# Performance work log

Measured on AMD Instinct MI355X. Metric: run time of the kernel, lower is better.

## Reference

```python
import jax, jax.numpy as jnp
import numpy as np

NUM_GROUPS = 64  # fixed for jit; indices are drawn in [0, 64)
H = 7
W = 7

def setup_inputs() -> dict:
    key = jax.random.key(0)
    k1, k2 = jax.random.split(key)
    x = jax.random.normal(k1, (2048, 512, 7, 7), dtype=jnp.float32)
    idx = jax.random.randint(k2, (2048,), 0, NUM_GROUPS, dtype=jnp.int32)
    return {"x": x, "tensor_list_assignmentindices": idx}

def reference(x, tensor_list_assignmentindices):
    # x: [N, M, H, W]; indices: [N] in [0, NUM_GROUPS)
    # Fused: sum over spatial dims first, then scatter-add per group.
    # Mathematically identical to scatter-then-spatial-sum in the original.
    x_sp = jnp.sum(x, axis=(2, 3))  # [N, M]
    group_sum = jax.ops.segment_sum(x_sp, tensor_list_assignmentindices,
                                    num_segments=NUM_GROUPS)  # [G, M]
    counts = jax.ops.segment_sum(jnp.ones((x.shape[0],), dtype=x.dtype),
                                 tensor_list_assignmentindices,
                                 num_segments=NUM_GROUPS)  # [G]
    out = group_sum / (counts[:, None] * (H * W))  # [G, M]
    return out[:, :, None, None]  # [G, M, 1, 1]
```

## Files before the change

kernel.cpp:

```cpp
#include <hip/hip_runtime.h>


#define N_SAMPLES 2048
#define M_CHANNELS 512
#define SPATIAL 49
#define GROUPS 64
#define SAMPLE_FLOATS (M_CHANNELS * SPATIAL)
#define WAVE_CH 64
#define WAVE_FLOATS (WAVE_CH * SPATIAL)

typedef __attribute__((address_space(1))) const void global_void;
typedef __attribute__((address_space(3))) void lds_void;

__global__ __launch_bounds__(256) void scatter_kernel(
    const float* __restrict__ x, const int* __restrict__ idx,
    float* __restrict__ accum) {
  __shared__ float lds[4 * WAVE_FLOATS];
  const int blk = blockIdx.x;
  const int n = blk >> 1;
  const int h = blk & 1;
  const int t = threadIdx.x;
  const int w = t >> 6;
  const int lane = t & 63;
  const int g = idx[n];

  const float* src = x + (size_t)n * SAMPLE_FLOATS
                       + (size_t)h * (SAMPLE_FLOATS / 2)
                       + (size_t)w * WAVE_FLOATS;
  float* ldsw = lds + w * WAVE_FLOATS;

#pragma unroll
  for (int k = 0; k < 12; ++k) {
    __builtin_amdgcn_global_load_lds(
        (global_void*)(src + (size_t)(k * 64 + lane) * 4),
        (lds_void*)(ldsw + k * 256), 16, 0, 0);
  }
  if (lane < 16) {
    __builtin_amdgcn_global_load_lds(
        (global_void*)(src + (size_t)(768 + lane) * 4),
        (lds_void*)(ldsw + 3072), 16, 0, 0);
  }

  asm volatile("s_waitcnt vmcnt(0)" ::: "memory");
  __builtin_amdgcn_sched_barrier(0);

  const float* row = ldsw + lane * SPATIAL;
  float s = 0.f;
#pragma unroll
  for (int i = 0; i < SPATIAL; ++i) s += row[i];

  atomicAdd(accum + (size_t)g * M_CHANNELS + h * (M_CHANNELS / 2)
                  + w * WAVE_CH + lane, s);
}

__global__ __launch_bounds__(512) void finalize_kernel(
    const int* __restrict__ idx, float* __restrict__ out) {
  const int g = blockIdx.x;
  const int t = threadIdx.x;

  __shared__ int cnt;
  if (t == 0) cnt = 0;
  __syncthreads();

  int local = 0;
#pragma unroll
  for (int i = 0; i < N_SAMPLES / 512; ++i)
    local += (idx[t + i * 512] == g) ? 1 : 0;
  atomicAdd(&cnt, local);
  __syncthreads();

  const float inv = 1.0f / ((float)cnt * (float)SPATIAL);
  out[(size_t)g * M_CHANNELS + t] *= inv;
}

extern "C" void kernel_launch(void* const* d_in, const int* in_sizes, int n_in,
                              void* d_out, int out_size, void* d_ws, size_t ws_size,
                              hipStream_t stream) {
  const float* x = (const float*)d_in[0];
  const int* idx = (const int*)d_in[1];
  float* out = (float*)d_out;

  hipMemsetAsync(out, 0, (size_t)GROUPS * M_CHANNELS * sizeof(float), stream);

  scatter_kernel<<<N_SAMPLES * 2, 256, 0, stream>>>(x, idx, out);
  finalize_kernel<<<GROUPS, M_CHANNELS, 0, stream>>>(idx, out);
}
```

Baseline: 278.5 us.

## Use persistent single-wave blocks with double-buffered LDS prefetch of channel chunks

Replaces the one-shot 4096-block scatter kernel with a persistent grid of 1536 single-wave blocks. Each block strides over 64-channel chunks and prefetches the next chunk into a second LDS buffer while reducing the current one, using a partial vmcnt wait. The spatial sum becomes a tree reduction to shorten the dependent add chain. The aim is to keep loads in flight continuously and hide latency, at the cost of fewer waves per CU and reliance on a precise vmcnt count. Without a barrier, the LDS buffer reuse depends on wave-local ordering.

New measurement: 281.1 us. Within noise of the previous version (+0.9%).

```diff
diff --git a/kernel.cpp b/kernel.cpp
--- a/kernel.cpp
+++ b/kernel.cpp
@@ -5,52 +5,67 @@
 #define M_CHANNELS 512
 #define SPATIAL 49
 #define GROUPS 64
-#define SAMPLE_FLOATS (M_CHANNELS * SPATIAL)
-#define WAVE_CH 64
-#define WAVE_FLOATS (WAVE_CH * SPATIAL)
+#define CHUNK_CH 64
+#define CHUNK_FLOATS (CHUNK_CH * SPATIAL)
+#define TOTAL_CHUNKS (N_SAMPLES * (M_CHANNELS / CHUNK_CH))
+#define GRID 1536
 
 typedef __attribute__((address_space(1))) const void global_void;
 typedef __attribute__((address_space(3))) void lds_void;
 
-__global__ __launch_bounds__(256) void scatter_kernel(
-    const float* __restrict__ x, const int* __restrict__ idx,
-    float* __restrict__ accum) {
-  __shared__ float lds[4 * WAVE_FLOATS];
-  const int blk = blockIdx.x;
-  const int n = blk >> 1;
-  const int h = blk & 1;
-  const int t = threadIdx.x;
-  const int w = t >> 6;
-  const int lane = t & 63;
-  const int g = idx[n];
-
-  const float* src = x + (size_t)n * SAMPLE_FLOATS
-                       + (size_t)h * (SAMPLE_FLOATS / 2)
-                       + (size_t)w * WAVE_FLOATS;
-  float* ldsw = lds + w * WAVE_FLOATS;
-
+__device__ __forceinline__ void stage_chunk(const float* __restrict__ src,
+                                            float* dst, int lane) {
 #pragma unroll
   for (int k = 0; k < 12; ++k) {
     __builtin_amdgcn_global_load_lds(
         (global_void*)(src + (size_t)(k * 64 + lane) * 4),
-        (lds_void*)(ldsw + k * 256), 16, 0, 0);
+        (lds_void*)(dst + k * 256), 16, 0, 0);
   }
   if (lane < 16) {
     __builtin_amdgcn_global_load_lds(
         (global_void*)(src + (size_t)(768 + lane) * 4),
-        (lds_void*)(ldsw + 3072), 16, 0, 0);
+        (lds_void*)(dst + 3072), 16, 0, 0);
   }
+}
 
+__device__ __forceinline__ void reduce_chunk(const float* ldsbuf, int lane,
+                                             const int* __restrict__ idx,
+                                             int chunk,
+                                             float* __restrict__ accum) {
+  const float* row = ldsbuf + lane * SPATIAL;
+  float v[SPATIAL];
+#pragma unroll
+  for (int i = 0; i < SPATIAL; ++i) v[i] = row[i];
+#pragma unroll
+  for (int s = 1; s < 64; s *= 2)
+#pragma unroll
+    for (int i = 0; i + s < SPATIAL; i += 2 * s) v[i] += v[i + s];
+  const int g = idx[chunk >> 3];
+  atomicAdd(accum + (size_t)g * M_CHANNELS + (chunk & 7) * CHUNK_CH + lane,
+            v[0]);
+}
+
+__global__ __launch_bounds__(64) void scatter_kernel(
+    const float* __restrict__ x, const int* __restrict__ idx,
+    float* __restrict__ accum) {
+  __shared__ float buf[2 * CHUNK_FLOATS];
+  const int lane = threadIdx.x;
+  int c = blockIdx.x;
+
+  stage_chunk(x + (size_t)c * CHUNK_FLOATS, buf, lane);
+  int cur = 0;
+  for (; c + GRID < TOTAL_CHUNKS; c += GRID) {
+    stage_chunk(x + (size_t)(c + GRID) * CHUNK_FLOATS,
+                buf + (cur ^ 1) * CHUNK_FLOATS, lane);
+    __builtin_amdgcn_sched_barrier(0);
+    asm volatile("s_waitcnt vmcnt(13)" ::: "memory");
+    __builtin_amdgcn_sched_barrier(0);
+    reduce_chunk(buf + cur * CHUNK_FLOATS, lane, idx, c, accum);
+    cur ^= 1;
+  }
   asm volatile("s_waitcnt vmcnt(0)" ::: "memory");
   __builtin_amdgcn_sched_barrier(0);
-
-  const float* row = ldsw + lane * SPATIAL;
-  float s = 0.f;
-#pragma unroll
-  for (int i = 0; i < SPATIAL; ++i) s += row[i];
-
-  atomicAdd(accum + (size_t)g * M_CHANNELS + h * (M_CHANNELS / 2)
-                  + w * WAVE_CH + lane, s);
+  reduce_chunk(buf + cur * CHUNK_FLOATS, lane, idx, c, accum);
 }
 
 __global__ __launch_bounds__(512) void finalize_kernel(
@@ -82,6 +97,6 @@
 
   hipMemsetAsync(out, 0, (size_t)GROUPS * M_CHANNELS * sizeof(float), stream);
 
-  scatter_kernel<<<N_SAMPLES * 2, 256, 0, stream>>>(x, idx, out);
+  scatter_kernel<<<GRID, 64, 0, stream>>>(x, idx, out);
   finalize_kernel<<<GROUPS, M_CHANNELS, 0, stream>>>(idx, out);
 }
```
